# Kernel tuning notes

Hardware: AMD Instinct MI355X
Metric: run time of the kernel (lower is better)

Reference implementation:

```python
import jax, jax.numpy as jnp
import numpy as np

ITERATIONS = 3


def setup_inputs() -> dict:
    key = jax.random.key(0)
    ks = jax.random.split(key, 12)
    B, S, H = 16, 128, 256
    N_LABELS, N_SLOTS = 22, 122
    sc = 0.02
    return {
        "h": jax.random.normal(ks[0], (B, S, H), jnp.float32),
        "c_slot": jax.random.normal(ks[1], (B, S, H), jnp.float32),
        "c_inte": jax.random.normal(ks[2], (B, H), jnp.float32),
        # weights stored as [in, out]; applied as x @ W (equivalent to torch Linear on random init)
        "W_SF": jax.random.normal(ks[3], (H, H), jnp.float32) * sc,
        "V_SF": jax.random.normal(ks[4], (H, H), jnp.float32) * sc,
        "V1_ID": jax.random.normal(ks[5], (H, H), jnp.float32) * sc,
        "V2_ID_w": jax.random.normal(ks[6], (H, H), jnp.float32) * sc,
        "V2_ID_b": jax.random.normal(ks[7], (H,), jnp.float32) * sc,
        "w_ID": jax.random.normal(ks[8], (H,), jnp.float32) * sc,
        "W_inte_ans": jax.random.normal(ks[9], (2 * H, N_LABELS), jnp.float32) * sc,
        "W_slot_ans": jax.random.normal(ks[10], (2 * H, N_SLOTS), jnp.float32) * sc,
    }


def reference(h, c_slot, c_inte, W_SF, V_SF, V1_ID, V2_ID_w, V2_ID_b, w_ID,
              W_inte_ans, W_slot_ans):
    B, S, H = h.shape
    diag = jnp.arange(S)
    r_inte = c_inte
    r_slot = c_slot  # placeholder; always overwritten in first iteration
    for _ in range(ITERATIONS):
        # SF step
        f = jnp.tanh(c_slot + (r_inte @ W_SF)[:, None, :])        # [B,S,H]
        f = (f @ V_SF).sum(axis=1)                                # [B,H]
        r_slot = f[:, None, :] * c_slot                           # [B,S,H]
        # ID step: pairwise additive attention, diagonal of row-softmax
        sf = r_slot @ V1_ID                                       # [B,S,H]
        hf = h @ V2_ID_w + V2_ID_b                                # [B,S,H]
        # scores[b,i,j] = w_ID . tanh(sf[b,i] + hf[b,j])
        scores = jnp.einsum('bijh,h->bij',
                            jnp.tanh(sf[:, :, None, :] + hf[:, None, :, :]),
                            w_ID)                                 # [B,S,S]
        probs = jax.nn.softmax(scores, axis=-1)                   # softmax over j
        alphas = probs[:, diag, diag]                             # [B,S]
        r = (r_slot * alphas[:, :, None]).sum(axis=1)             # [B,H]
        r_inte = r + c_inte
    intent_output = jnp.concatenate([r_inte, h[:, S - 1, :]], axis=-1) @ W_inte_ans
    slot_output = jnp.concatenate([h, r_slot], axis=-1) @ W_slot_ans
    return slot_output, intent_output
```

## Files before the change

kernel.cpp:

```cpp
#include <hip/hip_runtime.h>

#define Bn 16
#define Sn 128
#define Hn 256
#define NLn 22
#define NSn 122

#define K2c 2.8853900817779268f
#define L2Ec 1.4426950408889634f

__device__ __forceinline__ float fexp2(float x) { return __builtin_amdgcn_exp2f(x); }
__device__ __forceinline__ float frcp(float x) { return __builtin_amdgcn_rcpf(x); }

union F4 { float4 v; float f[4]; };

__device__ __forceinline__ void A_body(const float* __restrict__ c_slot,
                                       const float* __restrict__ c_inte,
                                       const float* __restrict__ W_SF,
                                       const float* __restrict__ V_SF,
                                       const float* __restrict__ alphas,
                                       float* __restrict__ g2,
                                       int b, int use_alpha,
                                       float* rL, float* fLq, float* aL,
                                       float (*pt)[Hn]) {
  const int tid = threadIdx.x;
  const int h = tid & (Hn - 1);
  const int kq = tid >> 8;

  if (use_alpha) {
    if (tid < Sn) aL[tid] = alphas[b * Sn + tid];
    __syncthreads();
    float ps = 0.f;
    #pragma unroll 8
    for (int s = kq * 32; s < kq * 32 + 32; ++s)
      ps += c_slot[(size_t)(b * Sn + s) * Hn + h] * aL[s];
    pt[kq][h] = ps;
    __syncthreads();
    if (!kq)
      rL[h] = c_inte[b * Hn + h] +
              g2[b * Hn + h] * (pt[0][h] + pt[1][h] + pt[2][h] + pt[3][h]);
  } else {
    if (!kq) rL[h] = c_inte[b * Hn + h];
  }
  __syncthreads();

  float pm = 0.f;
  #pragma unroll 8
  for (int k = kq * 64; k < kq * 64 + 64; ++k)
    pm += rL[k] * W_SF[(size_t)k * Hn + h];
  __syncthreads();
  pt[kq][h] = pm;
  __syncthreads();
  const float m = pt[0][h] + pt[1][h] + pt[2][h] + pt[3][h];
  const float em = fexp2(fminf(fmaxf(K2c * m, -60.f), 60.f));

  float pr = 0.f;
  #pragma unroll 8
  for (int s = kq * 32; s < kq * 32 + 32; ++s) {
    float zc = fminf(fmaxf(K2c * c_slot[(size_t)(b * Sn + s) * Hn + h], -60.f), 60.f);
    pr += frcp(fmaf(fexp2(zc), em, 1.f));
  }
  __syncthreads();
  pt[kq][h] = pr;
  __syncthreads();
  if (!kq) fLq[h] = (float)Sn - 2.f * (pt[0][h] + pt[1][h] + pt[2][h] + pt[3][h]);
  __syncthreads();

  float pg = 0.f;
  #pragma unroll 8
  for (int k = kq * 64; k < kq * 64 + 64; ++k)
    pg += fLq[k] * V_SF[(size_t)k * Hn + h];
  __syncthreads();
  pt[kq][h] = pg;
  __syncthreads();
  if (!kq)
    g2[b * Hn + h] = pt[0][h] + pt[1][h] + pt[2][h] + pt[3][h];
}

__global__ __launch_bounds__(1024) void k_hfA(const float* __restrict__ hp,
                                              const float* __restrict__ V2w,
                                              const float* __restrict__ V2b,
                                              const float* __restrict__ c_slot,
                                              const float* __restrict__ c_inte,
                                              const float* __restrict__ W_SF,
                                              const float* __restrict__ V_SF,
                                              float* __restrict__ ZT,
                                              float* __restrict__ g2) {
  __shared__ float xT[Hn][8];
  __shared__ float pp[3][Hn][8];
  __shared__ float rL[Hn];
  __shared__ float fLq[Hn];
  __shared__ float aL[Sn];
  __shared__ float pt[4][Hn];
  const int tid = threadIdx.x;
  const int blk = blockIdx.x;

  if (blk >= 256) {
    A_body(c_slot, c_inte, W_SF, V_SF, nullptr, g2, blk - 256, 0,
           rL, fLq, aL, pt);
    return;
  }

  const int r0 = blk * 8;
  const int b = r0 >> 7;
  const int j0 = r0 & (Sn - 1);
  const int h = tid & (Hn - 1);
  const int kh = tid >> 8;
  xT[h][kh * 2]     = hp[(size_t)(r0 + kh * 2) * Hn + h];
  xT[h][kh * 2 + 1] = hp[(size_t)(r0 + kh * 2 + 1) * Hn + h];
  __syncthreads();
  float acc[8] = {0.f, 0.f, 0.f, 0.f, 0.f, 0.f, 0.f, 0.f};
  #pragma unroll 8
  for (int k = kh * 64; k < kh * 64 + 64; ++k) {
    const float v = V2w[(size_t)k * Hn + h];
    F4 xa, xb;
    xa.v = *(const float4*)&xT[k][0];
    xb.v = *(const float4*)&xT[k][4];
    acc[0] += xa.f[0] * v; acc[1] += xa.f[1] * v;
    acc[2] += xa.f[2] * v; acc[3] += xa.f[3] * v;
    acc[4] += xb.f[0] * v; acc[5] += xb.f[1] * v;
    acc[6] += xb.f[2] * v; acc[7] += xb.f[3] * v;
  }
  if (kh) {
    F4 s0, s1;
    s0.f[0] = acc[0]; s0.f[1] = acc[1]; s0.f[2] = acc[2]; s0.f[3] = acc[3];
    s1.f[0] = acc[4]; s1.f[1] = acc[5]; s1.f[2] = acc[6]; s1.f[3] = acc[7];
    *(float4*)&pp[kh - 1][h][0] = s0.v;
    *(float4*)&pp[kh - 1][h][4] = s1.v;
  }
  __syncthreads();
  if (!kh) {
    const float bj = V2b[h];
    F4 o0, o1;
    #pragma unroll
    for (int i = 0; i < 8; ++i) {
      float z = K2c * (acc[i] + pp[0][h][i] + pp[1][h][i] + pp[2][h][i] + bj);
      z = fminf(fmaxf(z, -60.f), 60.f);
      if (i < 4) o0.f[i] = fexp2(z); else o1.f[i - 4] = fexp2(z);
    }
    *(float4*)&ZT[((size_t)b * Hn + h) * Sn + j0] = o0.v;
    *(float4*)&ZT[((size_t)b * Hn + h) * Sn + j0 + 4] = o1.v;
  }
}

__global__ __launch_bounds__(1024) void k_A(const float* __restrict__ c_slot,
                                            const float* __restrict__ c_inte,
                                            const float* __restrict__ W_SF,
                                            const float* __restrict__ V_SF,
                                            const float* __restrict__ alphas,
                                            float* __restrict__ g2) {
  __shared__ float rL[Hn];
  __shared__ float fLq[Hn];
  __shared__ float aL[Sn];
  __shared__ float pt[4][Hn];
  A_body(c_slot, c_inte, W_SF, V_SF, alphas, g2, blockIdx.x, 1,
         rL, fLq, aL, pt);
}

__global__ __launch_bounds__(1024) void k_C(const float* __restrict__ c_slot,
                                            const float* __restrict__ V1,
                                            const float* __restrict__ g2,
                                            const float* __restrict__ ZT,
                                            const float* __restrict__ wid,
                                            float* __restrict__ alphas) {
  __shared__ float bufA[Hn][4];
  __shared__ float bufB[Hn][4];
  __shared__ union {
    float pp[3][Hn][4];
    float red[7][4][Sn];
  } u;
  __shared__ float sc4[4][Sn];
  __shared__ float wL[Hn];

  const int tid = threadIdx.x;
  const int blk = blockIdx.x;
  const int b = blk >> 5;
  const int i0 = (blk & 31) * 4;
  const int h = tid & (Hn - 1);
  const int kq = tid >> 8;

  bufA[h][kq] = g2[b * Hn + h] * c_slot[(size_t)(b * Sn + i0 + kq) * Hn + h];
  if (tid < Hn) wL[tid] = wid[tid];
  __syncthreads();

  {
    float acc[4] = {0.f, 0.f, 0.f, 0.f};
    #pragma unroll 8
    for (int k = kq * 64; k < kq * 64 + 64; ++k) {
      const float v = V1[(size_t)k * Hn + h];
      F4 xa; xa.v = *(const float4*)&bufA[k][0];
      acc[0] += xa.f[0] * v; acc[1] += xa.f[1] * v;
      acc[2] += xa.f[2] * v; acc[3] += xa.f[3] * v;
    }
    if (kq) {
      F4 s0;
      s0.f[0] = acc[0]; s0.f[1] = acc[1]; s0.f[2] = acc[2]; s0.f[3] = acc[3];
      *(float4*)&u.pp[kq - 1][h][0] = s0.v;
    }
    __syncthreads();
    if (!kq) {
      #pragma unroll
      for (int i = 0; i < 4; ++i) {
        float z = K2c * (acc[i] + u.pp[0][h][i] + u.pp[1][h][i] + u.pp[2][h][i]);
        z = fminf(fmaxf(z, -60.f), 60.f);
        bufB[h][i] = fexp2(z);
      }
    }
  }
  __syncthreads();

  const int j = tid & (Sn - 1);
  const int hq = tid >> 7;
  float a4[4] = {0.f, 0.f, 0.f, 0.f};
  const float* zp = ZT + ((size_t)b * Hn + hq * 32) * Sn + j;
  #pragma unroll 4
  for (int hh = 0; hh < 32; ++hh) {
    const float z = zp[(size_t)hh * Sn];
    const float wh = wL[hq * 32 + hh];
    F4 ya; ya.v = *(const float4*)&bufB[hq * 32 + hh][0];
    a4[0] += wh * frcp(fmaf(ya.f[0], z, 1.f));
    a4[1] += wh * frcp(fmaf(ya.f[1], z, 1.f));
    a4[2] += wh * frcp(fmaf(ya.f[2], z, 1.f));
    a4[3] += wh * frcp(fmaf(ya.f[3], z, 1.f));
  }
  if (hq) {
    #pragma unroll
    for (int i = 0; i < 4; ++i) u.red[hq - 1][i][j] = a4[i];
  }
  __syncthreads();
  if (!hq) {
    #pragma unroll
    for (int i = 0; i < 4; ++i) {
      float tot = a4[i];
      #pragma unroll
      for (int r = 0; r < 7; ++r) tot += u.red[r][i][j];
      sc4[i][j] = -2.f * L2Ec * tot;
    }
  }
  __syncthreads();

  if (tid < 128) {
    const int row = tid >> 5;
    const int l5 = tid & 31;
    const float v0 = sc4[row][l5];
    const float v1 = sc4[row][l5 + 32];
    const float v2 = sc4[row][l5 + 64];
    const float v3 = sc4[row][l5 + 96];
    float mx = fmaxf(fmaxf(v0, v1), fmaxf(v2, v3));
    #pragma unroll
    for (int o = 16; o >= 1; o >>= 1) mx = fmaxf(mx, __shfl_xor(mx, o, 32));
    float sm = fexp2(v0 - mx) + fexp2(v1 - mx) + fexp2(v2 - mx) + fexp2(v3 - mx);
    #pragma unroll
    for (int o = 16; o >= 1; o >>= 1) sm += __shfl_xor(sm, o, 32);
    if (l5 == 0) {
      const int ig = i0 + row;
      alphas[b * Sn + ig] = fexp2(sc4[row][ig] - mx) * frcp(sm);
    }
  }
}

__global__ __launch_bounds__(512) void k_out(const float* __restrict__ hp,
                                             const float* __restrict__ c_slot,
                                             const float* __restrict__ c_inte,
                                             const float* __restrict__ g2,
                                             const float* __restrict__ alphas,
                                             const float* __restrict__ Wi,
                                             const float* __restrict__ Ws,
                                             float* __restrict__ outS,
                                             float* __restrict__ outI) {
  __shared__ float bufA[Hn][8];
  __shared__ float bufB[Hn][8];
  __shared__ float red[3][8][Sn];
  __shared__ float aL[Sn];
  __shared__ float cv[2 * Hn];
  __shared__ float ptA[2][Hn];
  __shared__ float ip[NLn][16];
  const int tid = threadIdx.x;
  const int blk = blockIdx.x;
  const int r0 = blk * 8;
  const int b2 = r0 >> 7;

  if (tid < Hn) {
    #pragma unroll
    for (int i = 0; i < 8; ++i) bufA[tid][i] = hp[(size_t)(r0 + i) * Hn + tid];
  } else {
    const int t = tid - Hn;
    const float gv = g2[b2 * Hn + t];
    #pragma unroll
    for (int i = 0; i < 8; ++i)
      bufB[t][i] = gv * c_slot[(size_t)(r0 + i) * Hn + t];
  }
  __syncthreads();
  const int jc = tid & 127;
  const int kq = tid >> 7;
  float acc[8] = {0.f, 0.f, 0.f, 0.f, 0.f, 0.f, 0.f, 0.f};
  if (jc < NSn) {
    const float (*xb)[8] = (kq < 2) ? bufA : bufB;
    const int kg0 = kq * 128;
    const int koff = (kq < 2) ? kg0 : kg0 - 256;
    #pragma unroll 8
    for (int u = 0; u < 128; ++u) {
      const float v = Ws[(size_t)(kg0 + u) * NSn + jc];
      F4 xa, xb4;
      xa.v = *(const float4*)&xb[koff + u][0];
      xb4.v = *(const float4*)&xb[koff + u][4];
      acc[0] += xa.f[0] * v; acc[1] += xa.f[1] * v;
      acc[2] += xa.f[2] * v; acc[3] += xa.f[3] * v;
      acc[4] += xb4.f[0] * v; acc[5] += xb4.f[1] * v;
      acc[6] += xb4.f[2] * v; acc[7] += xb4.f[3] * v;
    }
  }
  if (kq) {
    #pragma unroll
    for (int i = 0; i < 8; ++i) red[kq - 1][i][jc] = acc[i];
  }
  __syncthreads();
  if (!kq && jc < NSn) {
    #pragma unroll
    for (int i = 0; i < 8; ++i)
      outS[(size_t)(r0 + i) * NSn + jc] =
          acc[i] + red[0][i][jc] + red[1][i][jc] + red[2][i][jc];
  }

  if (blk < Bn) {
    const int b = blk;
    if (tid < Sn) aL[tid] = alphas[b * Sn + tid];
    __syncthreads();
    const int h = tid & (Hn - 1);
    const int k2 = tid >> 8;
    float ps = 0.f;
    #pragma unroll 8
    for (int s = k2 * 64; s < k2 * 64 + 64; ++s)
      ps += c_slot[(size_t)(b * Sn + s) * Hn + h] * aL[s];
    ptA[k2][h] = ps;
    __syncthreads();
    if (!k2) {
      cv[h] = c_inte[b * Hn + h] + g2[b * Hn + h] * (ptA[0][h] + ptA[1][h]);
      cv[Hn + h] = hp[(size_t)(b * Sn + Sn - 1) * Hn + h];
    }
    __syncthreads();
    if (tid < NLn * 16) {
      const int l = tid >> 4, c = tid & 15;
      float p = 0.f;
      #pragma unroll
      for (int k = c * 32; k < c * 32 + 32; ++k) p += cv[k] * Wi[k * NLn + l];
      ip[l][c] = p;
    }
    __syncthreads();
    if (tid < NLn) {
      float t = 0.f;
      #pragma unroll
      for (int c = 0; c < 16; ++c) t += ip[tid][c];
      outI[b * NLn + tid] = t;
    }
  }
}

extern "C" void kernel_launch(void* const* d_in, const int* in_sizes, int n_in,
                              void* d_out, int out_size, void* d_ws, size_t ws_size,
                              hipStream_t stream) {
  const float* hp     = (const float*)d_in[0];
  const float* c_slot = (const float*)d_in[1];
  const float* c_inte = (const float*)d_in[2];
  const float* W_SF   = (const float*)d_in[3];
  const float* V_SF   = (const float*)d_in[4];
  const float* V1     = (const float*)d_in[5];
  const float* V2w    = (const float*)d_in[6];
  const float* V2b    = (const float*)d_in[7];
  const float* wid    = (const float*)d_in[8];
  const float* Wi     = (const float*)d_in[9];
  const float* Ws     = (const float*)d_in[10];
  float* outS = (float*)d_out;
  float* outI = (float*)d_out + Bn * Sn * NSn;

  float* ws = (float*)d_ws;
  float* ZT     = ws;
  float* g2     = ZT + (size_t)Bn * Sn * Hn;
  float* alphas = g2 + Bn * Hn;

  hipLaunchKernelGGL(k_hfA, dim3(256 + Bn), dim3(1024), 0, stream,
                     hp, V2w, V2b, c_slot, c_inte, W_SF, V_SF, ZT, g2);
  hipLaunchKernelGGL(k_C, dim3(Bn * Sn / 4), dim3(1024), 0, stream,
                     c_slot, V1, g2, ZT, wid, alphas);
  for (int it = 1; it < 3; ++it) {
    hipLaunchKernelGGL(k_A, dim3(Bn), dim3(1024), 0, stream,
                       c_slot, c_inte, W_SF, V_SF, alphas, g2);
    hipLaunchKernelGGL(k_C, dim3(Bn * Sn / 4), dim3(1024), 0, stream,
                       c_slot, V1, g2, ZT, wid, alphas);
  }
  hipLaunchKernelGGL(k_out, dim3(Bn * Sn / 8), dim3(512), 0, stream,
                     hp, c_slot, c_inte, g2, alphas, Wi, Ws, outS, outI);
}
```

Baseline: 102.2 us.

## Fuse slot-output GEMM into final k_C launch as extra blocks

The slot-output projection (h and r_slot against W_slot_ans) moves out of the final output kernel and runs as 256 extra 1024-thread blocks appended to the last k_C launch, sharing a union of shared memory. That projection depends only on g2, which is already final at that point. A small k_int kernel with 16 blocks now computes only the intent output. The goal is to overlap the slot GEMM with the last attention step and shrink the tail kernel, at the cost of a larger shared-memory footprint per k_C block, which may lower occupancy.

Measured after the change: 107.8 us. 1.05x slower.

```diff
diff --git a/kernel.cpp b/kernel.cpp
--- a/kernel.cpp
+++ b/kernel.cpp
@@ -162,25 +162,85 @@
                                             const float* __restrict__ g2,
                                             const float* __restrict__ ZT,
                                             const float* __restrict__ wid,
-                                            float* __restrict__ alphas) {
-  __shared__ float bufA[Hn][4];
-  __shared__ float bufB[Hn][4];
-  __shared__ union {
-    float pp[3][Hn][4];
-    float red[7][4][Sn];
-  } u;
-  __shared__ float sc4[4][Sn];
-  __shared__ float wL[Hn];
+                                            float* __restrict__ alphas,
+                                            const float* __restrict__ hp,
+                                            const float* __restrict__ Ws,
+                                            float* __restrict__ outS) {
+  __shared__ union Shm {
+    struct {
+      float bufA[Hn][4];
+      float bufB[Hn][4];
+      union { float pp[3][Hn][4]; float red[7][4][Sn]; } u;
+      float sc4[4][Sn];
+      float wL[Hn];
+    } c;
+    struct {
+      float bufA[Hn][8];
+      float bufB[Hn][8];
+      float red[7][8][Sn];
+    } s;
+  } shm;
 
   const int tid = threadIdx.x;
   const int blk = blockIdx.x;
+
+  if (blk >= 512) {
+    const int sb = blk - 512;
+    const int r0 = sb * 8;
+    const int b2 = r0 >> 7;
+    const int h = tid & (Hn - 1);
+    const int q4 = tid >> 8;
+    const float gv = g2[b2 * Hn + h];
+    #pragma unroll
+    for (int i = 0; i < 2; ++i) {
+      const int row = q4 * 2 + i;
+      shm.s.bufA[h][row] = hp[(size_t)(r0 + row) * Hn + h];
+      shm.s.bufB[h][row] = gv * c_slot[(size_t)(r0 + row) * Hn + h];
+    }
+    __syncthreads();
+    const int jc = tid & 127;
+    const int k8 = tid >> 7;
+    float acc[8] = {0.f, 0.f, 0.f, 0.f, 0.f, 0.f, 0.f, 0.f};
+    if (jc < NSn) {
+      const float (*xb)[8] = (k8 < 4) ? shm.s.bufA : shm.s.bufB;
+      const int kg0 = k8 * 64;
+      const int koff = (k8 < 4) ? 0 : 256;
+      #pragma unroll 8
+      for (int u = 0; u < 64; ++u) {
+        const float v = Ws[(size_t)(kg0 + u) * NSn + jc];
+        F4 xa, xb4;
+        xa.v = *(const float4*)&xb[kg0 - koff + u][0];
+        xb4.v = *(const float4*)&xb[kg0 - koff + u][4];
+        acc[0] += xa.f[0] * v; acc[1] += xa.f[1] * v;
+        acc[2] += xa.f[2] * v; acc[3] += xa.f[3] * v;
+        acc[4] += xb4.f[0] * v; acc[5] += xb4.f[1] * v;
+        acc[6] += xb4.f[2] * v; acc[7] += xb4.f[3] * v;
+      }
+    }
+    if (k8) {
+      #pragma unroll
+      for (int i = 0; i < 8; ++i) shm.s.red[k8 - 1][i][jc] = acc[i];
+    }
+    __syncthreads();
+    if (!k8 && jc < NSn) {
+      #pragma unroll
+      for (int i = 0; i < 8; ++i) {
+        float tot = acc[i];
+        #pragma unroll
+        for (int r = 0; r < 7; ++r) tot += shm.s.red[r][i][jc];
+        outS[(size_t)(r0 + i) * NSn + jc] = tot;
+      }
+    }
+    return;
+  }
+
   const int b = blk >> 5;
   const int i0 = (blk & 31) * 4;
   const int h = tid & (Hn - 1);
   const int kq = tid >> 8;
 
-  bufA[h][kq] = g2[b * Hn + h] * c_slot[(size_t)(b * Sn + i0 + kq) * Hn + h];
-  if (tid < Hn) wL[tid] = wid[tid];
+  shm.c.bufA[h][kq] = g2[b * Hn + h] * c_slot[(size_t)(b * Sn + i0 + kq) * Hn + h];
+  if (tid < Hn) shm.c.wL[tid] = wid[tid];
   __syncthreads();
 
   {
@@ -188,22 +248,23 @@
     #pragma unroll 8
     for (int k = kq * 64; k < kq * 64 + 64; ++k) {
       const float v = V1[(size_t)k * Hn + h];
-      F4 xa; xa.v = *(const float4*)&bufA[k][0];
+      F4 xa; xa.v = *(const float4*)&shm.c.bufA[k][0];
       acc[0] += xa.f[0] * v; acc[1] += xa.f[1] * v;
       acc[2] += xa.f[2] * v; acc[3] += xa.f[3] * v;
     }
     if (kq) {
       F4 s0;
       s0.f[0] = acc[0]; s0.f[1] = acc[1]; s0.f[2] = acc[2]; s0.f[3] = acc[3];
-      *(float4*)&u.pp[kq - 1][h][0] = s0.v;
+      *(float4*)&shm.c.u.pp[kq - 1][h][0] = s0.v;
     }
     __syncthreads();
     if (!kq) {
       #pragma unroll
       for (int i = 0; i < 4; ++i) {
-        float z = K2c * (acc[i] + u.pp[0][h][i] + u.pp[1][h][i] + u.pp[2][h][i]);
+        float z = K2c * (acc[i] + shm.c.u.pp[0][h][i] + shm.c.u.pp[1][h][i] +
+                         shm.c.u.pp[2][h][i]);
         z = fminf(fmaxf(z, -60.f), 60.f);
-        bufB[h][i] = fexp2(z);
+        shm.c.bufB[h][i] = fexp2(z);
       }
     }
   }
@@ -216,8 +277,8 @@
   #pragma unroll 4
   for (int hh = 0; hh < 32; ++hh) {
     const float z = zp[(size_t)hh * Sn];
-    const float wh = wL[hq * 32 + hh];
-    F4 ya; ya.v = *(const float4*)&bufB[hq * 32 + hh][0];
+    const float wh = shm.c.wL[hq * 32 + hh];
+    F4 ya; ya.v = *(const float4*)&shm.c.bufB[hq * 32 + hh][0];
     a4[0] += wh * frcp(fmaf(ya.f[0], z, 1.f));
     a4[1] += wh * frcp(fmaf(ya.f[1], z, 1.f));
     a4[2] += wh * frcp(fmaf(ya.f[2], z, 1.f));
@@ -225,7 +286,7 @@
   }
   if (hq) {
     #pragma unroll
-    for (int i = 0; i < 4; ++i) u.red[hq - 1][i][j] = a4[i];
+    for (int i = 0; i < 4; ++i) shm.c.u.red[hq - 1][i][j] = a4[i];
   }
   __syncthreads();
   if (!hq) {
@@ -233,8 +294,8 @@
     for (int i = 0; i < 4; ++i) {
       float tot = a4[i];
       #pragma unroll
-      for (int r = 0; r < 7; ++r) tot += u.red[r][i][j];
-      sc4[i][j] = -2.f * L2Ec * tot;
+      for (int r = 0; r < 7; ++r) tot += shm.c.u.red[r][i][j];
+      shm.c.sc4[i][j] = -2.f * L2Ec * tot;
     }
   }
   __syncthreads();
@@ -242,10 +303,10 @@
   if (tid < 128) {
     const int row = tid >> 5;
     const int l5 = tid & 31;
-    const float v0 = sc4[row][l5];
-    const float v1 = sc4[row][l5 + 32];
-    const float v2 = sc4[row][l5 + 64];
-    const float v3 = sc4[row][l5 + 96];
+    const float v0 = shm.c.sc4[row][l5];
+    const float v1 = shm.c.sc4[row][l5 + 32];
+    const float v2 = shm.c.sc4[row][l5 + 64];
+    const float v3 = shm.c.sc4[row][l5 + 96];
     float mx = fmaxf(fmaxf(v0, v1), fmaxf(v2, v3));
     #pragma unroll
     for (int o = 16; o >= 1; o >>= 1) mx = fmaxf(mx, __shfl_xor(mx, o, 32));
@@ -254,105 +315,52 @@
     for (int o = 16; o >= 1; o >>= 1) sm += __shfl_xor(sm, o, 32);
     if (l5 == 0) {
       const int ig = i0 + row;
-      alphas[b * Sn + ig] = fexp2(sc4[row][ig] - mx) * frcp(sm);
-    }
-  }
-}
-
-__global__ __launch_bounds__(512) void k_out(const float* __restrict__ hp,
+      alphas[b * Sn + ig] = fexp2(shm.c.sc4[row][ig] - mx) * frcp(sm);
+    }
+  }
+}
+
+__global__ __launch_bounds__(512) void k_int(const float* __restrict__ hp,
                                              const float* __restrict__ c_slot,
                                              const float* __restrict__ c_inte,
                                              const float* __restrict__ g2,
                                              const float* __restrict__ alphas,
                                              const float* __restrict__ Wi,
-                                             const float* __restrict__ Ws,
-                                             float* __restrict__ outS,
                                              float* __restrict__ outI) {
-  __shared__ float bufA[Hn][8];
-  __shared__ float bufB[Hn][8];
-  __shared__ float red[3][8][Sn];
   __shared__ float aL[Sn];
   __shared__ float cv[2 * Hn];
   __shared__ float ptA[2][Hn];
   __shared__ float ip[NLn][16];
+  const int b = blockIdx.x;
   const int tid = threadIdx.x;
-  const int blk = blockIdx.x;
-  const int r0 = blk * 8;
-  const int b2 = r0 >> 7;
-
-  if (tid < Hn) {
-    #pragma unroll
-    for (int i = 0; i < 8; ++i) bufA[tid][i] = hp[(size_t)(r0 + i) * Hn + tid];
-  } else {
-    const int t = tid - Hn;
-    const float gv = g2[b2 * Hn + t];
-    #pragma unroll
-    for (int i = 0; i < 8; ++i)
-      bufB[t][i] = gv * c_slot[(size_t)(r0 + i) * Hn + t];
-  }
-  __syncthreads();
-  const int jc = tid & 127;
-  const int kq = tid >> 7;
-  float acc[8] = {0.f, 0.f, 0.f, 0.f, 0.f, 0.f, 0.f, 0.f};
-  if (jc < NSn) {
-    const float (*xb)[8] = (kq < 2) ? bufA : bufB;
-    const int kg0 = kq * 128;
-    const int koff = (kq < 2) ? kg0 : kg0 - 256;
-    #pragma unroll 8
-    for (int u = 0; u < 128; ++u) {
-      const float v = Ws[(size_t)(kg0 + u) * NSn + jc];
-      F4 xa, xb4;
-      xa.v = *(const float4*)&xb[koff + u][0];
-      xb4.v = *(const float4*)&xb[koff + u][4];
-      acc[0] += xa.f[0] * v; acc[1] += xa.f[1] * v;
-      acc[2] += xa.f[2] * v; acc[3] += xa.f[3] * v;
-      acc[4] += xb4.f[0] * v; acc[5] += xb4.f[1] * v;
-      acc[6] += xb4.f[2] * v; acc[7] += xb4.f[3] * v;
-    }
-  }
-  if (kq) {
-    #pragma unroll
-    for (int i = 0; i < 8; ++i) red[kq - 1][i][jc] = acc[i];
-  }
-  __syncthreads();
-  if (!kq && jc < NSn) {
-    #pragma unroll
-    for (int i = 0; i < 8; ++i)
-      outS[(size_t)(r0 + i) * NSn + jc] =
-          acc[i] + red[0][i][jc] + red[1][i][jc] + red[2][i][jc];
-  }
-
-  if (blk < Bn) {
-    const int b = blk;
-    if (tid < Sn) aL[tid] = alphas[b * Sn + tid];
-    __syncthreads();
-    const int h = tid & (Hn - 1);
-    const int k2 = tid >> 8;
-    float ps = 0.f;
-    #pragma unroll 8
-    for (int s = k2 * 64; s < k2 * 64 + 64; ++s)
-      ps += c_slot[(size_t)(b * Sn + s) * Hn + h] * aL[s];
-    ptA[k2][h] = ps;
-    __syncthreads();
-    if (!k2) {
-      cv[h] = c_inte[b * Hn + h] + g2[b * Hn + h] * (ptA[0][h] + ptA[1][h]);
-      cv[Hn + h] = hp[(size_t)(b * Sn + Sn - 1) * Hn + h];
-    }
-    __syncthreads();
-    if (tid < NLn * 16) {
-      const int l = tid >> 4, c = tid & 15;
-      float p = 0.f;
-      #pragma unroll
-      for (int k = c * 32; k < c * 32 + 32; ++k) p += cv[k] * Wi[k * NLn + l];
-      ip[l][c] = p;
-    }
-    __syncthreads();
-    if (tid < NLn) {
-      float t = 0.f;
-      #pragma unroll
-      for (int c = 0; c < 16; ++c) t += ip[tid][c];
-      outI[b * NLn + tid] = t;
-    }
+  if (tid < Sn) aL[tid] = alphas[b * Sn + tid];
+  __syncthreads();
+  const int h = tid & (Hn - 1);
+  const int k2 = tid >> 8;
+  float ps = 0.f;
+  #pragma unroll 8
+  for (int s = k2 * 64; s < k2 * 64 + 64; ++s)
+    ps += c_slot[(size_t)(b * Sn + s) * Hn + h] * aL[s];
+  ptA[k2][h] = ps;
+  __syncthreads();
+  if (!k2) {
+    cv[h] = c_inte[b * Hn + h] + g2[b * Hn + h] * (ptA[0][h] + ptA[1][h]);
+    cv[Hn + h] = hp[(size_t)(b * Sn + Sn - 1) * Hn + h];
+  }
+  __syncthreads();
+  if (tid < NLn * 16) {
+    const int l = tid >> 4, c = tid & 15;
+    float p = 0.f;
+    #pragma unroll
+    for (int k = c * 32; k < c * 32 + 32; ++k) p += cv[k] * Wi[k * NLn + l];
+    ip[l][c] = p;
+  }
+  __syncthreads();
+  if (tid < NLn) {
+    float t = 0.f;
+    #pragma unroll
+    for (int c = 0; c < 16; ++c) t += ip[tid][c];
+    outI[b * NLn + tid] = t;
   }
 }
 
@@ -380,14 +388,14 @@
 
   hipLaunchKernelGGL(k_hfA, dim3(256 + Bn), dim3(1024), 0, stream,
                      hp, V2w, V2b, c_slot, c_inte, W_SF, V_SF, ZT, g2);
-  hipLaunchKernelGGL(k_C, dim3(Bn * Sn / 4), dim3(1024), 0, stream,
-                     c_slot, V1, g2, ZT, wid, alphas);
+  hipLaunchKernelGGL(k_C, dim3(512), dim3(1024), 0, stream,
+                     c_slot, V1, g2, ZT, wid, alphas, hp, Ws, outS);
   for (int it = 1; it < 3; ++it) {
     hipLaunchKernelGGL(k_A, dim3(Bn), dim3(1024), 0, stream,
                        c_slot, c_inte, W_SF, V_SF, alphas, g2);
-    hipLaunchKernelGGL(k_C, dim3(Bn * Sn / 4), dim3(1024), 0, stream,
-                       c_slot, V1, g2, ZT, wid, alphas);
-  }
-  hipLaunchKernelGGL(k_out, dim3(Bn * Sn / 8), dim3(512), 0, stream,
-                     hp, c_slot, c_inte, g2, alphas, Wi, Ws, outS, outI);
-}
+    hipLaunchKernelGGL(k_C, dim3(it == 2 ? 768 : 512), dim3(1024), 0, stream,
+                       c_slot, V1, g2, ZT, wid, alphas, hp, Ws, outS);
+  }
+  hipLaunchKernelGGL(k_int, dim3(Bn), dim3(512), 0, stream,
+                     hp, c_slot, c_inte, g2, alphas, Wi, outI);
+}
```

## Fuse SF-update step into ID kernel tail via last-block atomic counter

Applied to the files above, without the earlier changes.

Removes the separate k_A launches by having the last of the 32 k_C blocks for each batch, detected with an atomic counter, run the SF update (A_body) for the next iteration. Alphas are written and read with agent-scope atomics so the tail block sees the other blocks' results. This saves two kernel launches and their gaps but adds a memset, atomics, and a serial tail on one block per batch.

Result: slower. 132.1 us (+29.2%).

```diff
diff --git a/kernel.cpp b/kernel.cpp
--- a/kernel.cpp
+++ b/kernel.cpp
@@ -18,9 +18,9 @@
                                        const float* __restrict__ c_inte,
                                        const float* __restrict__ W_SF,
                                        const float* __restrict__ V_SF,
-                                       const float* __restrict__ alphas,
+                                       const float* alphas,
                                        float* __restrict__ g2,
-                                       int b, int use_alpha,
+                                       int b, int use_alpha, int coh,
                                        float* rL, float* fLq, float* aL,
                                        float (*pt)[Hn]) {
   const int tid = threadIdx.x;
@@ -28,7 +28,10 @@
   const int kq = tid >> 8;
 
   if (use_alpha) {
-    if (tid < Sn) aL[tid] = alphas[b * Sn + tid];
+    if (tid < Sn)
+      aL[tid] = coh ? __hip_atomic_load(&alphas[b * Sn + tid],
+                                        __ATOMIC_RELAXED, __HIP_MEMORY_SCOPE_AGENT)
+                    : alphas[b * Sn + tid];
     __syncthreads();
     float ps = 0.f;
     #pragma unroll 8
@@ -96,7 +99,7 @@
   const int blk = blockIdx.x;
 
   if (blk >= 256) {
-    A_body(c_slot, c_inte, W_SF, V_SF, nullptr, g2, blk - 256, 0,
+    A_body(c_slot, c_inte, W_SF, V_SF, nullptr, g2, blk - 256, 0, 0,
            rL, fLq, aL, pt);
     return;
   }
@@ -143,34 +146,26 @@
   }
 }
 
-__global__ __launch_bounds__(1024) void k_A(const float* __restrict__ c_slot,
+__global__ __launch_bounds__(1024) void k_C(const float* __restrict__ c_slot,
+                                            const float* __restrict__ V1,
+                                            float* __restrict__ g2,
+                                            const float* __restrict__ ZT,
+                                            const float* __restrict__ wid,
+                                            float* alphas,
                                             const float* __restrict__ c_inte,
                                             const float* __restrict__ W_SF,
                                             const float* __restrict__ V_SF,
-                                            const float* __restrict__ alphas,
-                                            float* __restrict__ g2) {
-  __shared__ float rL[Hn];
-  __shared__ float fLq[Hn];
-  __shared__ float aL[Sn];
-  __shared__ float pt[4][Hn];
-  A_body(c_slot, c_inte, W_SF, V_SF, alphas, g2, blockIdx.x, 1,
-         rL, fLq, aL, pt);
-}
-
-__global__ __launch_bounds__(1024) void k_C(const float* __restrict__ c_slot,
-                                            const float* __restrict__ V1,
-                                            const float* __restrict__ g2,
-                                            const float* __restrict__ ZT,
-                                            const float* __restrict__ wid,
-                                            float* __restrict__ alphas) {
+                                            unsigned* cnt, int do_tail) {
   __shared__ float bufA[Hn][4];
   __shared__ float bufB[Hn][4];
   __shared__ union {
     float pp[3][Hn][4];
     float red[7][4][Sn];
+    struct { float rL[Hn]; float fLq[Hn]; float aL[Sn]; float pt[4][Hn]; } a;
   } u;
   __shared__ float sc4[4][Sn];
   __shared__ float wL[Hn];
+  __shared__ int lastFlag;
 
   const int tid = threadIdx.x;
   const int blk = blockIdx.x;
@@ -254,9 +249,24 @@
     for (int o = 16; o >= 1; o >>= 1) sm += __shfl_xor(sm, o, 32);
     if (l5 == 0) {
       const int ig = i0 + row;
-      alphas[b * Sn + ig] = fexp2(sc4[row][ig] - mx) * frcp(sm);
-    }
-  }
+      const float av = fexp2(sc4[row][ig] - mx) * frcp(sm);
+      __hip_atomic_store(&alphas[b * Sn + ig], av,
+                         __ATOMIC_RELAXED, __HIP_MEMORY_SCOPE_AGENT);
+    }
+  }
+
+  if (!do_tail) return;
+
+  __syncthreads();
+  if (tid == 0) {
+    unsigned old = __hip_atomic_fetch_add(&cnt[b], 1u, __ATOMIC_ACQ_REL,
+                                          __HIP_MEMORY_SCOPE_AGENT);
+    lastFlag = (old == 31u);
+  }
+  __syncthreads();
+  if (!lastFlag) return;
+  A_body(c_slot, c_inte, W_SF, V_SF, alphas, g2, b, 1, 1,
+         u.a.rL, u.a.fLq, u.a.aL, u.a.pt);
 }
 
 __global__ __launch_bounds__(512) void k_out(const float* __restrict__ hp,
@@ -374,20 +384,23 @@
   float* outI = (float*)d_out + Bn * Sn * NSn;
 
   float* ws = (float*)d_ws;
-  float* ZT     = ws;
-  float* g2     = ZT + (size_t)Bn * Sn * Hn;
-  float* alphas = g2 + Bn * Hn;
-
+  float* ZT      = ws;
+  float* g2      = ZT + (size_t)Bn * Sn * Hn;
+  float* alphas  = g2 + Bn * Hn;
+  unsigned* cnt  = (unsigned*)(alphas + Bn * Sn);
+
+  hipMemsetAsync(cnt, 0, 2 * Bn * sizeof(unsigned), stream);
   hipLaunchKernelGGL(k_hfA, dim3(256 + Bn), dim3(1024), 0, stream,
                      hp, V2w, V2b, c_slot, c_inte, W_SF, V_SF, ZT, g2);
-  hipLaunchKernelGGL(k_C, dim3(Bn * Sn / 4), dim3(1024), 0, stream,
-                     c_slot, V1, g2, ZT, wid, alphas);
-  for (int it = 1; it < 3; ++it) {
-    hipLaunchKernelGGL(k_A, dim3(Bn), dim3(1024), 0, stream,
-                       c_slot, c_inte, W_SF, V_SF, alphas, g2);
-    hipLaunchKernelGGL(k_C, dim3(Bn * Sn / 4), dim3(1024), 0, stream,
-                       c_slot, V1, g2, ZT, wid, alphas);
-  }
+  hipLaunchKernelGGL(k_C, dim3(512), dim3(1024), 0, stream,
+                     c_slot, V1, g2, ZT, wid, alphas, c_inte, W_SF, V_SF,
+                     cnt, 1);
+  hipLaunchKernelGGL(k_C, dim3(512), dim3(1024), 0, stream,
+                     c_slot, V1, g2, ZT, wid, alphas, c_inte, W_SF, V_SF,
+                     cnt + Bn, 1);
+  hipLaunchKernelGGL(k_C, dim3(512), dim3(1024), 0, stream,
+                     c_slot, V1, g2, ZT, wid, alphas, c_inte, W_SF, V_SF,
+                     nullptr, 0);
   hipLaunchKernelGGL(k_out, dim3(Bn * Sn / 8), dim3(512), 0, stream,
                      hp, c_slot, c_inte, g2, alphas, Wi, Ws, outS, outI);
 }
```
